# Optimization experiments

Measured on AMD Instinct MI355X. Metric: run time of the kernel, lower is better.

Reference implementation:

```python
import jax, jax.numpy as jnp
import numpy as np

B, S, D_IN = 32, 4096, 256
D, T, NB, K = 256, 256, 4, 5  # d_model, compressed_len, n_blocks, kernel_size
EPS = 1e-5


def setup_inputs() -> dict:
    key = jax.random.key(0)
    ks = jax.random.split(key, 20)
    x = jax.random.normal(ks[0], (B, S, D_IN), jnp.float32)
    # ragged valid-prefix lengths in [1, S]
    lengths = jax.random.randint(ks[1], (B,), 1, S + 1)
    mask = jnp.arange(S)[None, :] < lengths[:, None]  # bool [B,S]
    sc = 0.02
    inp = {
        'x': x,
        'mask': mask,
        'in_w': jax.random.normal(ks[2], (D_IN, D), jnp.float32) * sc,
        'in_b': jnp.zeros((D,), jnp.float32),
        'ln_g': jnp.ones((NB, D), jnp.float32),
        'ln_b': jnp.zeros((NB, D), jnp.float32),
        'dw_w': jax.random.normal(ks[3], (NB, D, 1, K), jnp.float32) * sc,
        'dw_b': jnp.zeros((NB, D), jnp.float32),
        'win_w': jax.random.normal(ks[4], (NB, D, 2 * D), jnp.float32) * sc,
        'win_b': jnp.zeros((NB, 2 * D), jnp.float32),
        'wout_w': jax.random.normal(ks[5], (NB, D, D), jnp.float32) * sc,
        'wout_b': jnp.zeros((NB, D), jnp.float32),
        'fn_g': jnp.ones((D,), jnp.float32),
        'fn_b': jnp.zeros((D,), jnp.float32),
    }
    return inp


def layer_norm(h, g, b):
    mu = jnp.mean(h, axis=-1, keepdims=True)
    var = jnp.mean((h - mu) ** 2, axis=-1, keepdims=True)
    return (h - mu) * jax.lax.rsqrt(var + EPS) * g + b


def compress(x, mask, target_len):
    # Vectorized equivalent of the per-sample F.interpolate(mode='linear',
    # align_corners=False) loop: src = (j+0.5)*(L/T) - 0.5, clamped, lerp.
    lengths = mask.astype(jnp.int32).sum(axis=1)  # [B]
    Lf = lengths.astype(x.dtype)
    j = jnp.arange(target_len, dtype=x.dtype)
    src = (j[None, :] + 0.5) * (Lf[:, None] / target_len) - 0.5  # [B,T]
    src = jnp.clip(src, 0.0, jnp.maximum(Lf[:, None] - 1.0, 0.0))
    i0 = jnp.floor(src).astype(jnp.int32)
    i1 = jnp.minimum(i0 + 1, jnp.maximum(lengths[:, None] - 1, 0))
    w = (src - i0.astype(x.dtype))[..., None]  # [B,T,1]
    gather = jax.vmap(lambda xb, ib: xb[ib])  # [S,D],[T] -> [T,D]
    out = (1.0 - w) * gather(x, i0) + w * gather(x, i1)  # [B,T,D]
    valid = lengths > 0
    out = jnp.where(valid[:, None, None], out, 0.0)
    comp_mask = jnp.broadcast_to(valid[:, None], (x.shape[0], target_len))
    return out, comp_mask


def conv_block(h, g, b, dww, dwb, winw, winb, woutw, woutb):
    residual = h
    hn = layer_norm(h, g, b)
    hc = jax.lax.conv_general_dilated(
        hn.transpose(0, 2, 1), dww, window_strides=(1,),
        padding=[(K // 2, K // 2)], dimension_numbers=('NCW', 'OIW', 'NCW'),
        feature_group_count=D)
    hc = hc.transpose(0, 2, 1) + dwb  # [B,T,D]
    gv = hc @ winw + winb
    gate, val = jnp.split(gv, 2, axis=-1)
    h2 = jax.nn.sigmoid(gate) * jax.nn.gelu(val, approximate=False)
    return residual + h2 @ woutw + woutb


def reference(x, mask, in_w, in_b, ln_g, ln_b, dw_w, dw_b, win_w, win_b,
              wout_w, wout_b, fn_g, fn_b):
    xc, comp_mask = compress(x, mask, T)
    h = xc @ in_w + in_b
    for i in range(NB):
        h = conv_block(h, ln_g[i], ln_b[i], dw_w[i], dw_b[i], win_w[i],
                       win_b[i], wout_w[i], wout_b[i])
    return layer_norm(h, fn_g, fn_b), comp_mask
```

## Files before the change

### kernel.cpp

```cpp
#include <hip/hip_runtime.h>
#include <math.h>

#define B_    32
#define S_    4096
#define DIN_  256
#define D_    256
#define T_    256
#define NB_   4
#define K_    5
#define EPS_  1e-5f
#define ROWS_ (B_ * T_)

#define MROWS 48
#define ASTR  264

typedef short  shortx8 __attribute__((ext_vector_type(8)));
typedef float  floatx4 __attribute__((ext_vector_type(4)));

__device__ __forceinline__ unsigned short f2bf(float f) {
    unsigned int u = __float_as_uint(f);
    u += 0x7FFFu + ((u >> 16) & 1u);
    return (unsigned short)(u >> 16);
}
__device__ __forceinline__ float bf2f(unsigned short h) {
    return __uint_as_float(((unsigned int)h) << 16);
}

__global__ void k_wt(const float* __restrict__ in_w, const float* __restrict__ win_w,
                     const float* __restrict__ wout_w,
                     unsigned short* __restrict__ wt_in, unsigned short* __restrict__ wt_win,
                     unsigned short* __restrict__ wt_wout) {
    int z = blockIdx.z;
    const float* src; unsigned short* dst; int N, Kd;
    if (z == 0)      { src = in_w;                                   dst = wt_in;                                   N = D_;     Kd = DIN_; }
    else if (z <= 4) { src = win_w  + (size_t)(z - 1) * D_ * 2 * D_; dst = wt_win  + (size_t)(z - 1) * 2 * D_ * D_; N = 2 * D_; Kd = D_; }
    else             { src = wout_w + (size_t)(z - 5) * D_ * D_;     dst = wt_wout + (size_t)(z - 5) * D_ * D_;     N = D_;     Kd = D_; }
    int bx = blockIdx.x * 32;
    int by = blockIdx.y * 32;
    if (bx >= N) return;
    __shared__ float tile[32][33];
    int tx = threadIdx.x & 31, ty = threadIdx.x >> 5;
#pragma unroll
    for (int i = 0; i < 32; i += 8)
        tile[ty + i][tx] = src[(size_t)(by + ty + i) * N + bx + tx];
    __syncthreads();
#pragma unroll
    for (int i = 0; i < 32; i += 8)
        dst[(size_t)(bx + ty + i) * Kd + by + tx] = f2bf(tile[tx][ty + i]);
}

template<bool INIT>
__device__ __forceinline__ void gemm_nk16(
    const unsigned short (*A)[ASTR], const unsigned short* __restrict__ wt,
    const float* __restrict__ bias, float (&hreg)[2][3][4],
    int w, int c16, int q)
{
#pragma unroll
    for (int nn = 0; nn < 2; ++nn) {
        int nt = w + nn * 8;
        const unsigned short* wp = wt + (size_t)(nt * 16 + c16) * 256 + q * 8;
        floatx4 acc[3] = {};
        shortx8 bcur = *(const shortx8*)wp;
#pragma unroll
        for (int kk = 0; kk < 8; ++kk) {
            shortx8 bnext = bcur;
            if (kk < 7) bnext = *(const shortx8*)(wp + (kk + 1) * 32);
#pragma unroll
            for (int mt = 0; mt < 3; ++mt) {
                shortx8 a = *(const shortx8*)&A[mt * 16 + c16][kk * 32 + q * 8];
                acc[mt] = __builtin_amdgcn_mfma_f32_16x16x32_bf16(a, bcur, acc[mt], 0, 0, 0);
            }
            bcur = bnext;
        }
        float ob = bias[nt * 16 + c16];
#pragma unroll
        for (int mt = 0; mt < 3; ++mt)
#pragma unroll
            for (int r = 0; r < 4; ++r) {
                float v = acc[mt][r] + ob;
                if (INIT) hreg[nn][mt][r] = v; else hreg[nn][mt][r] += v;
            }
    }
}

__device__ __forceinline__ void stats_pass(
    const float (&hreg)[2][3][4], float2* st,
    float (*rowS)[MROWS], float (*rowSS)[MROWS],
    int tid, int w, int c16, int q)
{
#pragma unroll
    for (int mt = 0; mt < 3; ++mt)
#pragma unroll
        for (int r = 0; r < 4; ++r) {
            float v0 = hreg[0][mt][r], v1 = hreg[1][mt][r];
            float s = v0 + v1, ss = v0 * v0 + v1 * v1;
#pragma unroll
            for (int off = 1; off < 16; off <<= 1) {
                s += __shfl_xor(s, off);
                ss += __shfl_xor(ss, off);
            }
            if (c16 == 0) {
                rowS[w][mt * 16 + q * 4 + r] = s;
                rowSS[w][mt * 16 + q * 4 + r] = ss;
            }
        }
    __syncthreads();
    if (tid < MROWS) {
        float s = 0.f, ss = 0.f;
#pragma unroll
        for (int i = 0; i < 8; ++i) { s += rowS[i][tid]; ss += rowSS[i][tid]; }
        float mu = s * (1.0f / D_);
        float var = ss * (1.0f / D_) - mu * mu;
        st[tid] = make_float2(mu, rsqrtf(var + EPS_));
    }
    __syncthreads();
}

__global__ __launch_bounds__(512, 2) void k_mega(
    const float* __restrict__ x, const unsigned int* __restrict__ mask_w,
    const unsigned short* __restrict__ wt_in, const float* __restrict__ in_b,
    const float* __restrict__ ln_g, const float* __restrict__ ln_b,
    const float* __restrict__ dw_w, const float* __restrict__ dw_b,
    const unsigned short* __restrict__ wt_win, const float* __restrict__ win_b,
    const unsigned short* __restrict__ wt_wout, const float* __restrict__ wout_b,
    const float* __restrict__ fn_g, const float* __restrict__ fn_b,
    float* __restrict__ out0, float* __restrict__ out1)
{
    __shared__ unsigned short buf0[MROWS][ASTR];
    __shared__ unsigned short buf1[MROWS][ASTR];
    __shared__ float2 st[MROWS];
    __shared__ float rowS[8][MROWS];
    __shared__ float rowSS[8][MROWS];
    __shared__ int redL[8];
    __shared__ int lenS;

    int tid = threadIdx.x;
    int w = tid >> 6, lane = tid & 63;
    int c16 = lane & 15, q = lane >> 4;
    int bid = blockIdx.x;
    int b = bid >> 3, seg = bid & 7;
    int t0 = seg * 32 - 8;
    if (t0 < 0) t0 = 0;
    if (t0 > T_ - MROWS) t0 = T_ - MROWS;
    int out_lo = seg * 32;

    float hreg[2][3][4];

    {
        int mode = 0;
        unsigned int w0 = mask_w[0];
        if (w0 == 0x3F800000u) mode = 2;
        else {
            bool u8 = false;
            for (int i = 0; i < 32; ++i) {
                if (mask_w[i * 1024] > 1u) { u8 = true; break; }
            }
            mode = u8 ? 1 : 0;
        }
        int s = 0;
        if (mode == 0) {
            const int* m = (const int*)mask_w;
            for (int i = tid; i < S_; i += 512) s += (m[(size_t)b * S_ + i] != 0);
        } else if (mode == 2) {
            const float* m = (const float*)mask_w;
            for (int i = tid; i < S_; i += 512) s += (m[(size_t)b * S_ + i] != 0.0f);
        } else {
            const unsigned char* m = (const unsigned char*)mask_w;
            for (int i = tid; i < S_; i += 512) s += (m[(size_t)b * S_ + i] != 0);
        }
#pragma unroll
        for (int off = 1; off < 64; off <<= 1) s += __shfl_xor(s, off);
        if (lane == 0) redL[w] = s;
        __syncthreads();
        if (tid == 0) {
            int tot = 0;
#pragma unroll
            for (int i = 0; i < 8; ++i) tot += redL[i];
            lenS = tot;
        }
        __syncthreads();
    }
    int L = lenS;

    {
        int ccol = tid & 255, r0 = tid >> 8;
        float Lf = (float)L;
        float hi = fmaxf(Lf - 1.0f, 0.0f);
        int L1 = max(L - 1, 0);
        const float* xb = x + (size_t)b * S_ * DIN_ + ccol;
#pragma unroll
        for (int e = 0; e < 24; ++e) {
            int row = r0 + e * 2;
            int t = t0 + row;
            float src = ((float)t + 0.5f) * (Lf * (1.0f / T_)) - 0.5f;
            src = fminf(fmaxf(src, 0.0f), hi);
            int i0 = (int)floorf(src);
            int i1 = min(i0 + 1, L1);
            float wf = src - (float)i0;
            float v0 = xb[(size_t)i0 * DIN_];
            float v1 = xb[(size_t)i1 * DIN_];
            buf0[row][ccol] = f2bf((1.0f - wf) * v0 + wf * v1);
        }
    }
    __syncthreads();

    gemm_nk16<true>(buf0, wt_in, in_b, hreg, w, c16, q);

    for (int li = 0; li < NB_; ++li) {
        const float* g_i = ln_g + li * D_;
        const float* b_i = ln_b + li * D_;
        const float* dww = dw_w + li * D_ * K_;
        const float* dwb = dw_b + li * D_;
        const unsigned short* ww = wt_win + (size_t)li * 2 * D_ * D_;
        const float* wb = win_b + li * 2 * D_;
        const unsigned short* ow = wt_wout + (size_t)li * D_ * D_;
        const float* ob = wout_b + li * D_;

        stats_pass(hreg, st, rowS, rowSS, tid, w, c16, q);

#pragma unroll
        for (int nn = 0; nn < 2; ++nn) {
            int col = (w + nn * 8) * 16 + c16;
            float gg = g_i[col], bb = b_i[col];
#pragma unroll
            for (int mt = 0; mt < 3; ++mt)
#pragma unroll
                for (int r = 0; r < 4; ++r) {
                    int row = mt * 16 + q * 4 + r;
                    float2 s = st[row];
                    buf0[row][col] = f2bf((hreg[nn][mt][r] - s.x) * s.y * gg + bb);
                }
        }
        __syncthreads();

        {
            int ccol = tid & 255, r0 = tid >> 8;
            float wk[K_];
#pragma unroll
            for (int k = 0; k < K_; ++k) wk[k] = dww[ccol * K_ + k];
            float cb = dwb[ccol];
#pragma unroll
            for (int e = 0; e < 24; ++e) {
                int row = r0 + e * 2;
                int t = t0 + row;
                float acc = cb;
#pragma unroll
                for (int k = 0; k < K_; ++k) {
                    int lr = row + k - 2, tt = t + k - 2;
                    if (lr >= 0 && lr < MROWS && tt >= 0 && tt < T_)
                        acc += bf2f(buf0[lr][ccol]) * wk[k];
                }
                buf1[row][ccol] = f2bf(acc);
            }
        }
        __syncthreads();

#pragma unroll
        for (int pp = 0; pp < 2; ++pp) {
            int p = w + pp * 8;
            const unsigned short* wg = ww + (size_t)(p * 16 + c16) * 256 + q * 8;
            const unsigned short* wv = wg + (size_t)256 * 256;
            floatx4 accg[3] = {}, accv[3] = {};
            shortx8 bg = *(const shortx8*)wg;
            shortx8 bv = *(const shortx8*)wv;
#pragma unroll
            for (int kk = 0; kk < 8; ++kk) {
                shortx8 bgn = bg, bvn = bv;
                if (kk < 7) {
                    bgn = *(const shortx8*)(wg + (kk + 1) * 32);
                    bvn = *(const shortx8*)(wv + (kk + 1) * 32);
                }
#pragma unroll
                for (int mt = 0; mt < 3; ++mt) {
                    shortx8 a = *(const shortx8*)&buf1[mt * 16 + c16][kk * 32 + q * 8];
                    accg[mt] = __builtin_amdgcn_mfma_f32_16x16x32_bf16(a, bg, accg[mt], 0, 0, 0);
                    accv[mt] = __builtin_amdgcn_mfma_f32_16x16x32_bf16(a, bv, accv[mt], 0, 0, 0);
                }
                bg = bgn; bv = bvn;
            }
            float biasg = wb[p * 16 + c16];
            float biasv = wb[256 + p * 16 + c16];
#pragma unroll
            for (int mt = 0; mt < 3; ++mt)
#pragma unroll
                for (int r = 0; r < 4; ++r) {
                    int row = mt * 16 + q * 4 + r;
                    float gate = accg[mt][r] + biasg;
                    float val  = accv[mt][r] + biasv;
                    float sg = 1.0f / (1.0f + expf(-gate));
                    float ge = 0.5f * val * (1.0f + erff(val * 0.70710678118654752f));
                    buf0[row][p * 16 + c16] = f2bf(sg * ge);
                }
        }
        __syncthreads();

        gemm_nk16<false>(buf0, ow, ob, hreg, w, c16, q);
    }

    stats_pass(hreg, st, rowS, rowSS, tid, w, c16, q);
#pragma unroll
    for (int nn = 0; nn < 2; ++nn) {
        int col = (w + nn * 8) * 16 + c16;
        float gg = fn_g[col], bb = fn_b[col];
#pragma unroll
        for (int mt = 0; mt < 3; ++mt)
#pragma unroll
            for (int r = 0; r < 4; ++r) {
                int row = mt * 16 + q * 4 + r;
                int t = t0 + row;
                int tl = t - out_lo;
                if (tl >= 0 && tl < 32) {
                    float2 s = st[row];
                    out0[((size_t)b * T_ + t) * D_ + col] =
                        (hreg[nn][mt][r] - s.x) * s.y * gg + bb;
                }
            }
    }
    if (tid < 32) out1[(size_t)b * T_ + out_lo + tid] = 1.0f;
}

extern "C" void kernel_launch(void* const* d_in, const int* in_sizes, int n_in,
                              void* d_out, int out_size, void* d_ws, size_t ws_size,
                              hipStream_t stream) {
    const float* x      = (const float*)d_in[0];
    const unsigned int* mask_w = (const unsigned int*)d_in[1];
    const float* in_w   = (const float*)d_in[2];
    const float* in_b   = (const float*)d_in[3];
    const float* ln_g   = (const float*)d_in[4];
    const float* ln_b   = (const float*)d_in[5];
    const float* dw_w   = (const float*)d_in[6];
    const float* dw_b   = (const float*)d_in[7];
    const float* win_w  = (const float*)d_in[8];
    const float* win_b  = (const float*)d_in[9];
    const float* wout_w = (const float*)d_in[10];
    const float* wout_b = (const float*)d_in[11];
    const float* fn_g   = (const float*)d_in[12];
    const float* fn_b   = (const float*)d_in[13];

    char* w8 = (char*)d_ws;
    unsigned short* wt_in   = (unsigned short*)w8;
    unsigned short* wt_win  = wt_in  + (size_t)D_ * DIN_;
    unsigned short* wt_wout = wt_win + (size_t)NB_ * 2 * D_ * D_;

    float* out0 = (float*)d_out;
    float* out1 = out0 + (size_t)ROWS_ * D_;

    k_wt<<<dim3(16, 8, 9), 256, 0, stream>>>(in_w, win_w, wout_w, wt_in, wt_win, wt_wout);
    k_mega<<<256, 512, 0, stream>>>(x, mask_w, wt_in, in_b, ln_g, ln_b, dw_w, dw_b,
                                    wt_win, win_b, wt_wout, wout_b, fn_g, fn_b,
                                    out0, out1);
}
```

Before: 292.5 us.

## Split sequence into 16-row tiles, precompute lengths, use fast tanh-GELU

Doubles the grid so each block computes 16 output rows using a 32-row window, raising occupancy and spreading work over more CUs. Mask length counting moves into the setup kernel, conv boundaries use zero-padded rows instead of per-tap bounds checks, weight fragments are preloaded per tile, and the gate/value GEMM is split from the activation. Exact erf GELU is replaced with a tanh approximation computed via exp. This trades more halo recompute and weight reloads per output for parallelism, at some accuracy risk.

```diff
diff --git a/kernel.cpp b/kernel.cpp
--- a/kernel.cpp
+++ b/kernel.cpp
@@ -11,7 +11,8 @@
 #define EPS_  1e-5f
 #define ROWS_ (B_ * T_)
 
-#define MROWS 48
+#define MROWS 32
+#define GROWS 36
 #define ASTR  264
 
 typedef short  shortx8 __attribute__((ext_vector_type(8)));
@@ -26,11 +27,47 @@
     return __uint_as_float(((unsigned int)h) << 16);
 }
 
-__global__ void k_wt(const float* __restrict__ in_w, const float* __restrict__ win_w,
-                     const float* __restrict__ wout_w,
-                     unsigned short* __restrict__ wt_in, unsigned short* __restrict__ wt_win,
-                     unsigned short* __restrict__ wt_wout) {
+__global__ void k_setup(const float* __restrict__ in_w, const float* __restrict__ win_w,
+                        const float* __restrict__ wout_w, const unsigned int* __restrict__ mask_w,
+                        unsigned short* __restrict__ wt_in, unsigned short* __restrict__ wt_win,
+                        unsigned short* __restrict__ wt_wout, int* __restrict__ lengths) {
     int z = blockIdx.z;
+    int tid = threadIdx.x;
+
+    if (z == 9) {
+        int b = blockIdx.y * 16 + blockIdx.x;
+        if (b >= B_) return;
+        int mode = 0;
+        unsigned int w0 = mask_w[0];
+        if (w0 == 0x3F800000u) mode = 2;
+        else {
+            bool u8 = false;
+            for (int i = 0; i < 32; ++i)
+                if (mask_w[i * 1024] > 1u) { u8 = true; break; }
+            mode = u8 ? 1 : 0;
+        }
+        int s = 0;
+        if (mode == 0) {
+            const int* m = (const int*)mask_w;
+            for (int i = tid; i < S_; i += 256) s += (m[(size_t)b * S_ + i] != 0);
+        } else if (mode == 2) {
+            const float* m = (const float*)mask_w;
+            for (int i = tid; i < S_; i += 256) s += (m[(size_t)b * S_ + i] != 0.0f);
+        } else {
+            const unsigned char* m = (const unsigned char*)mask_w;
+            for (int i = tid; i < S_; i += 256) s += (m[(size_t)b * S_ + i] != 0);
+        }
+        __shared__ int sm[256];
+        sm[tid] = s;
+        __syncthreads();
+        for (int off = 128; off > 0; off >>= 1) {
+            if (tid < off) sm[tid] += sm[tid + off];
+            __syncthreads();
+        }
+        if (tid == 0) lengths[b] = sm[0];
+        return;
+    }
+
     const float* src; unsigned short* dst; int N, Kd;
     if (z == 0)      { src = in_w;                                   dst = wt_in;                                   N = D_;     Kd = DIN_; }
     else if (z <= 4) { src = win_w  + (size_t)(z - 1) * D_ * 2 * D_; dst = wt_win  + (size_t)(z - 1) * 2 * D_ * D_; N = 2 * D_; Kd = D_; }
@@ -39,7 +76,7 @@
     int by = blockIdx.y * 32;
     if (bx >= N) return;
     __shared__ float tile[32][33];
-    int tx = threadIdx.x & 31, ty = threadIdx.x >> 5;
+    int tx = tid & 31, ty = tid >> 5;
 #pragma unroll
     for (int i = 0; i < 32; i += 8)
         tile[ty + i][tx] = src[(size_t)(by + ty + i) * N + bx + tx];
@@ -50,31 +87,30 @@
 }
 
 template<bool INIT>
-__device__ __forceinline__ void gemm_nk16(
+__device__ __forceinline__ void gemm2(
     const unsigned short (*A)[ASTR], const unsigned short* __restrict__ wt,
-    const float* __restrict__ bias, float (&hreg)[2][3][4],
+    const float* __restrict__ bias, float (&hreg)[2][2][4],
     int w, int c16, int q)
 {
 #pragma unroll
     for (int nn = 0; nn < 2; ++nn) {
         int nt = w + nn * 8;
         const unsigned short* wp = wt + (size_t)(nt * 16 + c16) * 256 + q * 8;
-        floatx4 acc[3] = {};
-        shortx8 bcur = *(const shortx8*)wp;
+        shortx8 Bf[8];
+#pragma unroll
+        for (int kk = 0; kk < 8; ++kk) Bf[kk] = *(const shortx8*)(wp + kk * 32);
+        floatx4 acc[2] = {};
 #pragma unroll
         for (int kk = 0; kk < 8; ++kk) {
-            shortx8 bnext = bcur;
-            if (kk < 7) bnext = *(const shortx8*)(wp + (kk + 1) * 32);
-#pragma unroll
-            for (int mt = 0; mt < 3; ++mt) {
-                shortx8 a = *(const shortx8*)&A[mt * 16 + c16][kk * 32 + q * 8];
-                acc[mt] = __builtin_amdgcn_mfma_f32_16x16x32_bf16(a, bcur, acc[mt], 0, 0, 0);
-            }
-            bcur = bnext;
+#pragma unroll
+            for (int mt = 0; mt < 2; ++mt) {
+                shortx8 a = *(const shortx8*)&A[2 + mt * 16 + c16][kk * 32 + q * 8];
+                acc[mt] = __builtin_amdgcn_mfma_f32_16x16x32_bf16(a, Bf[kk], acc[mt], 0, 0, 0);
+            }
         }
         float ob = bias[nt * 16 + c16];
 #pragma unroll
-        for (int mt = 0; mt < 3; ++mt)
+        for (int mt = 0; mt < 2; ++mt)
 #pragma unroll
             for (int r = 0; r < 4; ++r) {
                 float v = acc[mt][r] + ob;
@@ -84,12 +120,12 @@
 }
 
 __device__ __forceinline__ void stats_pass(
-    const float (&hreg)[2][3][4], float2* st,
+    const float (&hreg)[2][2][4], float2* st,
     float (*rowS)[MROWS], float (*rowSS)[MROWS],
     int tid, int w, int c16, int q)
 {
 #pragma unroll
-    for (int mt = 0; mt < 3; ++mt)
+    for (int mt = 0; mt < 2; ++mt)
 #pragma unroll
         for (int r = 0; r < 4; ++r) {
             float v0 = hreg[0][mt][r], v1 = hreg[1][mt][r];
@@ -116,8 +152,8 @@
     __syncthreads();
 }
 
-__global__ __launch_bounds__(512, 2) void k_mega(
-    const float* __restrict__ x, const unsigned int* __restrict__ mask_w,
+__global__ __launch_bounds__(512, 4) void k_mega(
+    const float* __restrict__ x, const int* __restrict__ lengths,
     const unsigned short* __restrict__ wt_in, const float* __restrict__ in_b,
     const float* __restrict__ ln_g, const float* __restrict__ ln_b,
     const float* __restrict__ dw_w, const float* __restrict__ dw_b,
@@ -126,61 +162,24 @@
     const float* __restrict__ fn_g, const float* __restrict__ fn_b,
     float* __restrict__ out0, float* __restrict__ out1)
 {
-    __shared__ unsigned short buf0[MROWS][ASTR];
-    __shared__ unsigned short buf1[MROWS][ASTR];
+    __shared__ unsigned short buf0[GROWS][ASTR];
+    __shared__ unsigned short buf1[GROWS][ASTR];
     __shared__ float2 st[MROWS];
     __shared__ float rowS[8][MROWS];
     __shared__ float rowSS[8][MROWS];
-    __shared__ int redL[8];
-    __shared__ int lenS;
 
     int tid = threadIdx.x;
     int w = tid >> 6, lane = tid & 63;
     int c16 = lane & 15, q = lane >> 4;
     int bid = blockIdx.x;
-    int b = bid >> 3, seg = bid & 7;
-    int t0 = seg * 32 - 8;
+    int b = bid >> 4, seg = bid & 15;
+    int t0 = seg * 16 - 8;
     if (t0 < 0) t0 = 0;
     if (t0 > T_ - MROWS) t0 = T_ - MROWS;
-    int out_lo = seg * 32;
-
-    float hreg[2][3][4];
-
-    {
-        int mode = 0;
-        unsigned int w0 = mask_w[0];
-        if (w0 == 0x3F800000u) mode = 2;
-        else {
-            bool u8 = false;
-            for (int i = 0; i < 32; ++i) {
-                if (mask_w[i * 1024] > 1u) { u8 = true; break; }
-            }
-            mode = u8 ? 1 : 0;
-        }
-        int s = 0;
-        if (mode == 0) {
-            const int* m = (const int*)mask_w;
-            for (int i = tid; i < S_; i += 512) s += (m[(size_t)b * S_ + i] != 0);
-        } else if (mode == 2) {
-            const float* m = (const float*)mask_w;
-            for (int i = tid; i < S_; i += 512) s += (m[(size_t)b * S_ + i] != 0.0f);
-        } else {
-            const unsigned char* m = (const unsigned char*)mask_w;
-            for (int i = tid; i < S_; i += 512) s += (m[(size_t)b * S_ + i] != 0);
-        }
-#pragma unroll
-        for (int off = 1; off < 64; off <<= 1) s += __shfl_xor(s, off);
-        if (lane == 0) redL[w] = s;
-        __syncthreads();
-        if (tid == 0) {
-            int tot = 0;
-#pragma unroll
-            for (int i = 0; i < 8; ++i) tot += redL[i];
-            lenS = tot;
-        }
-        __syncthreads();
-    }
-    int L = lenS;
+    int out_lo = seg * 16;
+
+    float hreg[2][2][4];
+    int L = lengths[b];
 
     {
         int ccol = tid & 255, r0 = tid >> 8;
@@ -189,7 +188,7 @@
         int L1 = max(L - 1, 0);
         const float* xb = x + (size_t)b * S_ * DIN_ + ccol;
 #pragma unroll
-        for (int e = 0; e < 24; ++e) {
+        for (int e = 0; e < 16; ++e) {
             int row = r0 + e * 2;
             int t = t0 + row;
             float src = ((float)t + 0.5f) * (Lf * (1.0f / T_)) - 0.5f;
@@ -199,12 +198,12 @@
             float wf = src - (float)i0;
             float v0 = xb[(size_t)i0 * DIN_];
             float v1 = xb[(size_t)i1 * DIN_];
-            buf0[row][ccol] = f2bf((1.0f - wf) * v0 + wf * v1);
+            buf0[2 + row][ccol] = f2bf((1.0f - wf) * v0 + wf * v1);
         }
     }
     __syncthreads();
 
-    gemm_nk16<true>(buf0, wt_in, in_b, hreg, w, c16, q);
+    gemm2<true>(buf0, wt_in, in_b, hreg, w, c16, q);
 
     for (int li = 0; li < NB_; ++li) {
         const float* g_i = ln_g + li * D_;
@@ -223,13 +222,22 @@
             int col = (w + nn * 8) * 16 + c16;
             float gg = g_i[col], bb = b_i[col];
 #pragma unroll
-            for (int mt = 0; mt < 3; ++mt)
+            for (int mt = 0; mt < 2; ++mt)
 #pragma unroll
                 for (int r = 0; r < 4; ++r) {
                     int row = mt * 16 + q * 4 + r;
                     float2 s = st[row];
-                    buf0[row][col] = f2bf((hreg[nn][mt][r] - s.x) * s.y * gg + bb);
+                    buf0[2 + row][col] = f2bf((hreg[nn][mt][r] - s.x) * s.y * gg + bb);
                 }
+        }
+        {
+            int idx = tid;
+#pragma unroll
+            for (int zz = 0; zz < 2; ++zz, idx += 512) {
+                int gr = idx >> 8;
+                int p = (gr < 2) ? gr : gr + 32;
+                buf0[p][idx & 255] = 0;
+            }
         }
         __syncthreads();
 
@@ -240,61 +248,59 @@
             for (int k = 0; k < K_; ++k) wk[k] = dww[ccol * K_ + k];
             float cb = dwb[ccol];
 #pragma unroll
-            for (int e = 0; e < 24; ++e) {
+            for (int e = 0; e < 16; ++e) {
                 int row = r0 + e * 2;
-                int t = t0 + row;
                 float acc = cb;
 #pragma unroll
-                for (int k = 0; k < K_; ++k) {
-                    int lr = row + k - 2, tt = t + k - 2;
-                    if (lr >= 0 && lr < MROWS && tt >= 0 && tt < T_)
-                        acc += bf2f(buf0[lr][ccol]) * wk[k];
+                for (int k = 0; k < K_; ++k)
+                    acc += bf2f(buf0[row + k][ccol]) * wk[k];
+                buf1[2 + row][ccol] = f2bf(acc);
+            }
+        }
+        __syncthreads();
+
+        float gvreg[4][2][4];
+#pragma unroll
+        for (int nn = 0; nn < 4; ++nn) {
+            int nt = w + nn * 8;
+            const unsigned short* wp = ww + (size_t)(nt * 16 + c16) * 256 + q * 8;
+            shortx8 Bf[8];
+#pragma unroll
+            for (int kk = 0; kk < 8; ++kk) Bf[kk] = *(const shortx8*)(wp + kk * 32);
+            floatx4 acc[2] = {};
+#pragma unroll
+            for (int kk = 0; kk < 8; ++kk) {
+#pragma unroll
+                for (int mt = 0; mt < 2; ++mt) {
+                    shortx8 a = *(const shortx8*)&buf1[2 + mt * 16 + c16][kk * 32 + q * 8];
+                    acc[mt] = __builtin_amdgcn_mfma_f32_16x16x32_bf16(a, Bf[kk], acc[mt], 0, 0, 0);
                 }
-                buf1[row][ccol] = f2bf(acc);
-            }
+            }
+            float bb = wb[nt * 16 + c16];
+#pragma unroll
+            for (int mt = 0; mt < 2; ++mt)
+#pragma unroll
+                for (int r = 0; r < 4; ++r) gvreg[nn][mt][r] = acc[mt][r] + bb;
+        }
+
+#pragma unroll
+        for (int pp = 0; pp < 2; ++pp) {
+            int col = (w + pp * 8) * 16 + c16;
+#pragma unroll
+            for (int mt = 0; mt < 2; ++mt)
+#pragma unroll
+                for (int r = 0; r < 4; ++r) {
+                    float gate = gvreg[pp][mt][r];
+                    float val  = gvreg[pp + 2][mt][r];
+                    float sg = 1.0f / (1.0f + __expf(-gate));
+                    float u = 1.5957691216f * (val + 0.044715f * val * val * val);
+                    float ge = val / (1.0f + __expf(-u));
+                    buf0[2 + mt * 16 + q * 4 + r][col] = f2bf(sg * ge);
+                }
         }
         __syncthreads();
 
-#pragma unroll
-        for (int pp = 0; pp < 2; ++pp) {
-            int p = w + pp * 8;
-            const unsigned short* wg = ww + (size_t)(p * 16 + c16) * 256 + q * 8;
-            const unsigned short* wv = wg + (size_t)256 * 256;
-            floatx4 accg[3] = {}, accv[3] = {};
-            shortx8 bg = *(const shortx8*)wg;
-            shortx8 bv = *(const shortx8*)wv;
-#pragma unroll
-            for (int kk = 0; kk < 8; ++kk) {
-                shortx8 bgn = bg, bvn = bv;
-                if (kk < 7) {
-                    bgn = *(const shortx8*)(wg + (kk + 1) * 32);
-                    bvn = *(const shortx8*)(wv + (kk + 1) * 32);
-                }
-#pragma unroll
-                for (int mt = 0; mt < 3; ++mt) {
-                    shortx8 a = *(const shortx8*)&buf1[mt * 16 + c16][kk * 32 + q * 8];
-                    accg[mt] = __builtin_amdgcn_mfma_f32_16x16x32_bf16(a, bg, accg[mt], 0, 0, 0);
-                    accv[mt] = __builtin_amdgcn_mfma_f32_16x16x32_bf16(a, bv, accv[mt], 0, 0, 0);
-                }
-                bg = bgn; bv = bvn;
-            }
-            float biasg = wb[p * 16 + c16];
-            float biasv = wb[256 + p * 16 + c16];
-#pragma unroll
-            for (int mt = 0; mt < 3; ++mt)
-#pragma unroll
-                for (int r = 0; r < 4; ++r) {
-                    int row = mt * 16 + q * 4 + r;
-                    float gate = accg[mt][r] + biasg;
-                    float val  = accv[mt][r] + biasv;
-                    float sg = 1.0f / (1.0f + expf(-gate));
-                    float ge = 0.5f * val * (1.0f + erff(val * 0.70710678118654752f));
-                    buf0[row][p * 16 + c16] = f2bf(sg * ge);
-                }
-        }
-        __syncthreads();
-
-        gemm_nk16<false>(buf0, ow, ob, hreg, w, c16, q);
+        gemm2<false>(buf0, ow, ob, hreg, w, c16, q);
     }
 
     stats_pass(hreg, st, rowS, rowSS, tid, w, c16, q);
@@ -303,20 +309,20 @@
         int col = (w + nn * 8) * 16 + c16;
         float gg = fn_g[col], bb = fn_b[col];
 #pragma unroll
-        for (int mt = 0; mt < 3; ++mt)
+        for (int mt = 0; mt < 2; ++mt)
 #pragma unroll
             for (int r = 0; r < 4; ++r) {
                 int row = mt * 16 + q * 4 + r;
                 int t = t0 + row;
                 int tl = t - out_lo;
-                if (tl >= 0 && tl < 32) {
+                if (tl >= 0 && tl < 16) {
                     float2 s = st[row];
                     out0[((size_t)b * T_ + t) * D_ + col] =
                         (hreg[nn][mt][r] - s.x) * s.y * gg + bb;
                 }
             }
     }
-    if (tid < 32) out1[(size_t)b * T_ + out_lo + tid] = 1.0f;
+    if (tid < 16) out1[(size_t)b * T_ + out_lo + tid] = 1.0f;
 }
 
 extern "C" void kernel_launch(void* const* d_in, const int* in_sizes, int n_in,
@@ -341,12 +347,14 @@
     unsigned short* wt_in   = (unsigned short*)w8;
     unsigned short* wt_win  = wt_in  + (size_t)D_ * DIN_;
     unsigned short* wt_wout = wt_win + (size_t)NB_ * 2 * D_ * D_;
+    int* lengths = (int*)(w8 + (4u << 20));
 
     float* out0 = (float*)d_out;
     float* out1 = out0 + (size_t)ROWS_ * D_;
 
-    k_wt<<<dim3(16, 8, 9), 256, 0, stream>>>(in_w, win_w, wout_w, wt_in, wt_win, wt_wout);
-    k_mega<<<256, 512, 0, stream>>>(x, mask_w, wt_in, in_b, ln_g, ln_b, dw_w, dw_b,
+    k_setup<<<dim3(16, 8, 10), 256, 0, stream>>>(in_w, win_w, wout_w, mask_w,
+                                                 wt_in, wt_win, wt_wout, lengths);
+    k_mega<<<512, 512, 0, stream>>>(x, lengths, wt_in, in_b, ln_g, ln_b, dw_w, dw_b,
                                     wt_win, win_b, wt_wout, wout_b, fn_g, fn_b,
                                     out0, out1);
 }
```

Result: slower. 312.8 us (+7.0%).
